# Kernel optimization log

Measured on AMD Instinct MI355X. Metric: run time of the kernel, lower is better.

The kernel has to match this reference:

```python
import jax, jax.numpy as jnp
import numpy as np

BLKPT = 1.0     # black-point percentile
WHTPT = 99.0    # white-point percentile
MAX_MULT = 1.5  # cap on brightening multiplier


def setup_inputs() -> dict:
    key = jax.random.key(0)
    # [B, 3, H, W] image in [0, 1]
    image = jax.random.uniform(key, (16, 3, 1024, 1024), dtype=jnp.float32)
    # standard BT.601 RGB->YUV matrix (module buffer RGB2YUV)
    rgb2yuv = jnp.array([[0.299, 0.587, 0.114],
                         [-0.14713, -0.28886, 0.436],
                         [0.615, -0.51499, -0.10001]], dtype=jnp.float32)
    return {"image": image, "rgb2yuv": rgb2yuv}


def reference(image, rgb2yuv):
    # Only the Y (luma) channel of the YUV conversion is consumed, so we
    # contract with the first matrix row instead of materializing full YUV.
    y = jnp.einsum('j,bjhw->bhw', rgb2yuv[0], image)        # [B, H, W]
    yf = y.reshape(y.shape[0], -1)                          # [B, H*W]
    blkpt = jnp.percentile(yf, BLKPT, axis=1)               # [B]
    whtpt = jnp.percentile(yf, WHTPT, axis=1)               # [B]
    mult = jnp.minimum(1.0 / (whtpt - blkpt), MAX_MULT)     # max_mult > 0 branch
    blkpt = blkpt[:, None, None, None]
    mult = mult[:, None, None, None]
    return jnp.clip((image - blkpt) * mult, 0.0, 1.0)
```

## Files before the change

### kernel.cpp

```cpp
#include <hip/hip_runtime.h>
#include <hip/hip_bf16.h>

#define NPIX (1024 * 1024)
#define NBATCH 16
#define NBINS 8192
#define SUBPB 64

typedef float vfloat4 __attribute__((ext_vector_type(4)));

__global__ void zero_kernel(unsigned int* __restrict__ ghist) {
    int i = blockIdx.x * blockDim.x + threadIdx.x;
    int n = NBATCH * NBINS;
    for (; i < n; i += gridDim.x * blockDim.x) ghist[i] = 0u;
}

__global__ __launch_bounds__(256) void hist_kernel(
        const float* __restrict__ img,
        const float* __restrict__ rgb2yuv,
        unsigned int* __restrict__ ghist) {
    __shared__ unsigned int lh[NBINS];
    for (int i = threadIdx.x; i < NBINS; i += blockDim.x) lh[i] = 0;
    const float c0 = rgb2yuv[0];
    const float c1 = rgb2yuv[1];
    const float c2 = rgb2yuv[2];
    __syncthreads();

    const int b = blockIdx.x / SUBPB;
    const int s = blockIdx.x % SUBPB;
    const int pixPerBlock = NPIX / SUBPB;
    const size_t base = (size_t)b * 3 * NPIX + (size_t)s * pixPerBlock;

    const float4* r4 = (const float4*)(img + base);
    const float4* g4 = (const float4*)(img + base + NPIX);
    const float4* b4 = (const float4*)(img + base + 2 * (size_t)NPIX);
    const int n4 = pixPerBlock / 4;

    const float scale = (float)NBINS;
    for (int i = threadIdx.x; i < n4; i += blockDim.x) {
        float4 R = r4[i];
        float4 G = g4[i];
        float4 B = b4[i];
        float y0 = c0 * R.x + c1 * G.x + c2 * B.x;
        float y1 = c0 * R.y + c1 * G.y + c2 * B.y;
        float y2 = c0 * R.z + c1 * G.z + c2 * B.z;
        float y3 = c0 * R.w + c1 * G.w + c2 * B.w;
        int i0 = min(NBINS - 1, max(0, (int)(y0 * scale)));
        int i1 = min(NBINS - 1, max(0, (int)(y1 * scale)));
        int i2 = min(NBINS - 1, max(0, (int)(y2 * scale)));
        int i3 = min(NBINS - 1, max(0, (int)(y3 * scale)));
        atomicAdd(&lh[i0], 1u);
        atomicAdd(&lh[i1], 1u);
        atomicAdd(&lh[i2], 1u);
        atomicAdd(&lh[i3], 1u);
    }
    __syncthreads();

    unsigned int* dst = ghist + (size_t)b * NBINS;
    for (int i = threadIdx.x; i < NBINS; i += blockDim.x) {
        unsigned int v = lh[i];
        if (v) atomicAdd(&dst[i], v);
    }
}

__global__ __launch_bounds__(1024) void scan_kernel(
        const unsigned int* __restrict__ ghist,
        float* __restrict__ stats) {
    __shared__ unsigned int hist[NBINS];
    __shared__ unsigned int segsum[1024];
    __shared__ float vals[4];

    const int b = blockIdx.x;
    const int t = threadIdx.x;

    for (int i = t; i < NBINS; i += 1024)
        hist[i] = ghist[(size_t)b * NBINS + i];
    __syncthreads();

    const int BPT = NBINS / 1024;
    unsigned int ss = 0;
#pragma unroll
    for (int j = 0; j < BPT; ++j) ss += hist[t * BPT + j];
    segsum[t] = ss;
    __syncthreads();

    for (int off = 1; off < 1024; off <<= 1) {
        unsigned int v = segsum[t];
        unsigned int add = (t >= off) ? segsum[t - off] : 0u;
        __syncthreads();
        segsum[t] = v + add;
        __syncthreads();
    }

    const unsigned int cumincl = segsum[t];
    const unsigned int cumbefore = (t > 0) ? segsum[t - 1] : 0u;

    const unsigned int ranks[4] = {10485u, 10486u, 1038089u, 1038090u};
#pragma unroll
    for (int q = 0; q < 4; ++q) {
        unsigned int r = ranks[q];
        if (r >= cumbefore && r < cumincl) {
            unsigned int running = cumbefore;
#pragma unroll
            for (int j = 0; j < BPT; ++j) {
                unsigned int c = hist[t * BPT + j];
                if (r < running + c) {
                    float v = ((float)(t * BPT + j) +
                               ((float)(r - running) + 0.5f) / (float)c) *
                              (1.0f / (float)NBINS);
                    vals[q] = v;
                    break;
                }
                running += c;
            }
        }
    }
    __syncthreads();

    if (t == 0) {
        float blk = 0.25f * vals[0] + 0.75f * vals[1];
        float wht = 0.75f * vals[2] + 0.25f * vals[3];
        float mult = fminf(1.0f / (wht - blk), 1.5f);
        stats[b * 2 + 0] = blk;
        stats[b * 2 + 1] = mult;
    }
}

__global__ __launch_bounds__(256) void apply_kernel(
        const float* __restrict__ img,
        const float* __restrict__ stats,
        float* __restrict__ out) {
    const int blocksPerBatch = (3 * NPIX / 4) / 1024;
    const int b = blockIdx.x / blocksPerBatch;
    const int c = blockIdx.x % blocksPerBatch;
    const float blk = stats[b * 2 + 0];
    const float mult = stats[b * 2 + 1];

    const vfloat4* in4 =
        (const vfloat4*)(img + (size_t)b * 3 * NPIX) + (size_t)c * 1024;
    vfloat4* out4 = (vfloat4*)(out + (size_t)b * 3 * NPIX) + (size_t)c * 1024;

#pragma unroll
    for (int i = 0; i < 4; ++i) {
        int idx = i * 256 + threadIdx.x;
        vfloat4 v = in4[idx];
        v.x = fminf(fmaxf((v.x - blk) * mult, 0.0f), 1.0f);
        v.y = fminf(fmaxf((v.y - blk) * mult, 0.0f), 1.0f);
        v.z = fminf(fmaxf((v.z - blk) * mult, 0.0f), 1.0f);
        v.w = fminf(fmaxf((v.w - blk) * mult, 0.0f), 1.0f);
        __builtin_nontemporal_store(v, out4 + idx);
    }
}

extern "C" void kernel_launch(void* const* d_in, const int* in_sizes, int n_in,
                              void* d_out, int out_size, void* d_ws, size_t ws_size,
                              hipStream_t stream) {
    const float* img = (const float*)d_in[0];
    const float* rgb2yuv = (const float*)d_in[1];
    float* out = (float*)d_out;

    float* stats = (float*)d_ws;
    unsigned int* ghist = (unsigned int*)((char*)d_ws + 256);

    zero_kernel<<<256, 256, 0, stream>>>(ghist);
    hist_kernel<<<NBATCH * SUBPB, 256, 0, stream>>>(img, rgb2yuv, ghist);
    scan_kernel<<<NBATCH, 1024, 0, stream>>>(ghist, stats);

    const int applyBlocks = NBATCH * ((3 * NPIX / 4) / 1024);
    apply_kernel<<<applyBlocks, 256, 0, stream>>>(img, stats, out);
}
```

Measured before the change: 382.0 us.

## Replace global histogram atomics with per-block partial histograms reduced in scan

Each histogram block now writes its private shared-memory histogram to its own slice of global memory with plain vector stores, instead of merging into a per-batch histogram with global atomics. The scan kernel sums the partial histograms itself, so the zeroing kernel and one launch go away. Block count is halved and threads per block doubled to keep the same pixel coverage. The cost is that the scan kernel, which runs only 16 blocks, must read 32 partial histograms per batch. Workspace use also grows to 512 histograms of 8192 bins.

```diff
diff --git a/kernel.cpp b/kernel.cpp
--- a/kernel.cpp
+++ b/kernel.cpp
@@ -1,25 +1,19 @@
 #include <hip/hip_runtime.h>
-#include <hip/hip_bf16.h>
 
 #define NPIX (1024 * 1024)
 #define NBATCH 16
 #define NBINS 8192
-#define SUBPB 64
+#define SUBPB 32
+#define HTHREADS 512
 
 typedef float vfloat4 __attribute__((ext_vector_type(4)));
 
-__global__ void zero_kernel(unsigned int* __restrict__ ghist) {
-    int i = blockIdx.x * blockDim.x + threadIdx.x;
-    int n = NBATCH * NBINS;
-    for (; i < n; i += gridDim.x * blockDim.x) ghist[i] = 0u;
-}
-
-__global__ __launch_bounds__(256) void hist_kernel(
+__global__ __launch_bounds__(HTHREADS) void hist_kernel(
         const float* __restrict__ img,
         const float* __restrict__ rgb2yuv,
         unsigned int* __restrict__ ghist) {
     __shared__ unsigned int lh[NBINS];
-    for (int i = threadIdx.x; i < NBINS; i += blockDim.x) lh[i] = 0;
+    for (int i = threadIdx.x; i < NBINS; i += HTHREADS) lh[i] = 0;
     const float c0 = rgb2yuv[0];
     const float c1 = rgb2yuv[1];
     const float c2 = rgb2yuv[2];
@@ -36,7 +30,7 @@
     const int n4 = pixPerBlock / 4;
 
     const float scale = (float)NBINS;
-    for (int i = threadIdx.x; i < n4; i += blockDim.x) {
+    for (int i = threadIdx.x; i < n4; i += HTHREADS) {
         float4 R = r4[i];
         float4 G = g4[i];
         float4 B = b4[i];
@@ -55,11 +49,9 @@
     }
     __syncthreads();
 
-    unsigned int* dst = ghist + (size_t)b * NBINS;
-    for (int i = threadIdx.x; i < NBINS; i += blockDim.x) {
-        unsigned int v = lh[i];
-        if (v) atomicAdd(&dst[i], v);
-    }
+    uint4* dst = (uint4*)(ghist + (size_t)blockIdx.x * NBINS);
+    const uint4* src = (const uint4*)lh;
+    for (int i = threadIdx.x; i < NBINS / 4; i += HTHREADS) dst[i] = src[i];
 }
 
 __global__ __launch_bounds__(1024) void scan_kernel(
@@ -72,14 +64,21 @@
     const int b = blockIdx.x;
     const int t = threadIdx.x;
 
-    for (int i = t; i < NBINS; i += 1024)
-        hist[i] = ghist[(size_t)b * NBINS + i];
-    __syncthreads();
-
-    const int BPT = NBINS / 1024;
+    unsigned int a[8] = {0u, 0u, 0u, 0u, 0u, 0u, 0u, 0u};
+    for (int s = 0; s < SUBPB; ++s) {
+        const uint4* p =
+            (const uint4*)(ghist + ((size_t)b * SUBPB + s) * NBINS + t * 8);
+        uint4 v0 = p[0];
+        uint4 v1 = p[1];
+        a[0] += v0.x; a[1] += v0.y; a[2] += v0.z; a[3] += v0.w;
+        a[4] += v1.x; a[5] += v1.y; a[6] += v1.z; a[7] += v1.w;
+    }
     unsigned int ss = 0;
 #pragma unroll
-    for (int j = 0; j < BPT; ++j) ss += hist[t * BPT + j];
+    for (int j = 0; j < 8; ++j) {
+        hist[t * 8 + j] = a[j];
+        ss += a[j];
+    }
     segsum[t] = ss;
     __syncthreads();
 
@@ -95,6 +94,7 @@
     const unsigned int cumbefore = (t > 0) ? segsum[t - 1] : 0u;
 
     const unsigned int ranks[4] = {10485u, 10486u, 1038089u, 1038090u};
+    const int BPT = NBINS / 1024;
 #pragma unroll
     for (int q = 0; q < 4; ++q) {
         unsigned int r = ranks[q];
@@ -161,8 +161,7 @@
     float* stats = (float*)d_ws;
     unsigned int* ghist = (unsigned int*)((char*)d_ws + 256);
 
-    zero_kernel<<<256, 256, 0, stream>>>(ghist);
-    hist_kernel<<<NBATCH * SUBPB, 256, 0, stream>>>(img, rgb2yuv, ghist);
+    hist_kernel<<<NBATCH * SUBPB, HTHREADS, 0, stream>>>(img, rgb2yuv, ghist);
     scan_kernel<<<NBATCH, 1024, 0, stream>>>(ghist, stats);
 
     const int applyBlocks = NBATCH * ((3 * NPIX / 4) / 1024);
```

Result: no change. 379.4 us (-0.7%).

## Fuse percentile scan into histogram kernel via last-block-done pattern

Applied to the files above, without the earlier changes.

Removes the separate scan kernel: each histogram block increments a per-batch counter after merging its shared histogram, and the last block for each batch does the prefix scan and writes blackpoint and multiplier. The histogram launch changes to fewer sub-blocks per batch (32) with 512 threads, and the scan uses vectorized uint4 loads into the reused shared histogram. The apply kernel swaps nontemporal stores for plain stores. This saves one kernel launch and its ramp, at the cost of serialized tail work in the last block and extra fences.

```diff
diff --git a/kernel.cpp b/kernel.cpp
--- a/kernel.cpp
+++ b/kernel.cpp
@@ -1,25 +1,30 @@
 #include <hip/hip_runtime.h>
-#include <hip/hip_bf16.h>
 
 #define NPIX (1024 * 1024)
 #define NBATCH 16
 #define NBINS 8192
-#define SUBPB 64
+#define SUBPB 32
+#define HTHREADS 512
 
 typedef float vfloat4 __attribute__((ext_vector_type(4)));
 
-__global__ void zero_kernel(unsigned int* __restrict__ ghist) {
+__global__ void zero_kernel(unsigned int* __restrict__ g, int n) {
     int i = blockIdx.x * blockDim.x + threadIdx.x;
-    int n = NBATCH * NBINS;
-    for (; i < n; i += gridDim.x * blockDim.x) ghist[i] = 0u;
+    for (; i < n; i += gridDim.x * blockDim.x) g[i] = 0u;
 }
 
-__global__ __launch_bounds__(256) void hist_kernel(
+__global__ __launch_bounds__(HTHREADS) void hist_kernel(
         const float* __restrict__ img,
         const float* __restrict__ rgb2yuv,
-        unsigned int* __restrict__ ghist) {
+        unsigned int* __restrict__ ghist,
+        unsigned int* __restrict__ flags,
+        float* __restrict__ stats) {
     __shared__ unsigned int lh[NBINS];
-    for (int i = threadIdx.x; i < NBINS; i += blockDim.x) lh[i] = 0;
+    __shared__ unsigned int segsum[HTHREADS];
+    __shared__ float vals[4];
+    __shared__ int isLast;
+
+    for (int i = threadIdx.x; i < NBINS; i += HTHREADS) lh[i] = 0;
     const float c0 = rgb2yuv[0];
     const float c1 = rgb2yuv[1];
     const float c2 = rgb2yuv[2];
@@ -36,7 +41,7 @@
     const int n4 = pixPerBlock / 4;
 
     const float scale = (float)NBINS;
-    for (int i = threadIdx.x; i < n4; i += blockDim.x) {
+    for (int i = threadIdx.x; i < n4; i += HTHREADS) {
         float4 R = r4[i];
         float4 G = g4[i];
         float4 B = b4[i];
@@ -56,34 +61,34 @@
     __syncthreads();
 
     unsigned int* dst = ghist + (size_t)b * NBINS;
-    for (int i = threadIdx.x; i < NBINS; i += blockDim.x) {
+    for (int i = threadIdx.x; i < NBINS; i += HTHREADS) {
         unsigned int v = lh[i];
         if (v) atomicAdd(&dst[i], v);
     }
-}
 
-__global__ __launch_bounds__(1024) void scan_kernel(
-        const unsigned int* __restrict__ ghist,
-        float* __restrict__ stats) {
-    __shared__ unsigned int hist[NBINS];
-    __shared__ unsigned int segsum[1024];
-    __shared__ float vals[4];
+    __threadfence();
+    if (threadIdx.x == 0) {
+        unsigned int old = atomicAdd(&flags[b], 1u);
+        isLast = (old == SUBPB - 1u) ? 1 : 0;
+    }
+    __syncthreads();
+    if (!isLast) return;
+    __threadfence();
 
-    const int b = blockIdx.x;
     const int t = threadIdx.x;
-
-    for (int i = t; i < NBINS; i += 1024)
-        hist[i] = ghist[(size_t)b * NBINS + i];
-    __syncthreads();
-
-    const int BPT = NBINS / 1024;
+    const uint4* gh = (const uint4*)(ghist + (size_t)b * NBINS);
+    uint4* lh4 = (uint4*)lh;
     unsigned int ss = 0;
 #pragma unroll
-    for (int j = 0; j < BPT; ++j) ss += hist[t * BPT + j];
+    for (int k = 0; k < 4; ++k) {
+        uint4 h = gh[t * 4 + k];
+        lh4[t * 4 + k] = h;
+        ss += h.x + h.y + h.z + h.w;
+    }
     segsum[t] = ss;
     __syncthreads();
 
-    for (int off = 1; off < 1024; off <<= 1) {
+    for (int off = 1; off < HTHREADS; off <<= 1) {
         unsigned int v = segsum[t];
         unsigned int add = (t >= off) ? segsum[t - off] : 0u;
         __syncthreads();
@@ -95,14 +100,14 @@
     const unsigned int cumbefore = (t > 0) ? segsum[t - 1] : 0u;
 
     const unsigned int ranks[4] = {10485u, 10486u, 1038089u, 1038090u};
+    const int BPT = NBINS / HTHREADS;
 #pragma unroll
     for (int q = 0; q < 4; ++q) {
         unsigned int r = ranks[q];
         if (r >= cumbefore && r < cumincl) {
             unsigned int running = cumbefore;
-#pragma unroll
             for (int j = 0; j < BPT; ++j) {
-                unsigned int c = hist[t * BPT + j];
+                unsigned int c = lh[t * BPT + j];
                 if (r < running + c) {
                     float v = ((float)(t * BPT + j) +
                                ((float)(r - running) + 0.5f) / (float)c) *
@@ -147,7 +152,7 @@
         v.y = fminf(fmaxf((v.y - blk) * mult, 0.0f), 1.0f);
         v.z = fminf(fmaxf((v.z - blk) * mult, 0.0f), 1.0f);
         v.w = fminf(fmaxf((v.w - blk) * mult, 0.0f), 1.0f);
-        __builtin_nontemporal_store(v, out4 + idx);
+        out4[idx] = v;
     }
 }
 
@@ -160,11 +165,11 @@
 
     float* stats = (float*)d_ws;
     unsigned int* ghist = (unsigned int*)((char*)d_ws + 256);
+    unsigned int* flags = ghist + NBATCH * NBINS;
 
-    zero_kernel<<<256, 256, 0, stream>>>(ghist);
-    hist_kernel<<<NBATCH * SUBPB, 256, 0, stream>>>(img, rgb2yuv, ghist);
-    scan_kernel<<<NBATCH, 1024, 0, stream>>>(ghist, stats);
-
+    zero_kernel<<<512, 256, 0, stream>>>(ghist, NBATCH * NBINS + NBATCH);
+    hist_kernel<<<NBATCH * SUBPB, HTHREADS, 0, stream>>>(img, rgb2yuv, ghist,
+                                                         flags, stats);
     const int applyBlocks = NBATCH * ((3 * NPIX / 4) / 1024);
     apply_kernel<<<applyBlocks, 256, 0, stream>>>(img, stats, out);
 }
```

Measured after the change: 454.2 us. 1.19x slower.
